# Kernel tuning notes

Measured on AMD Instinct MI355X. Metric: run time of the kernel, lower is better.

## Reference

```python
import jax, jax.numpy as jnp
import numpy as np

K_NEIGHBOURS = 40  # includes self; self is dropped after top-k


def setup_inputs() -> dict:
    key = jax.random.key(0)
    ks = jax.random.split(key, 4)
    B, V, F_in = 4, 4096, 64
    P, S, F_out = 64, 4, 64
    x = jax.random.normal(ks[0], (B, V, F_in), dtype=jnp.float32)
    Wf = jax.random.normal(ks[1], (F_in, P), dtype=jnp.float32) / np.sqrt(F_in)
    bf = jnp.zeros((P,), dtype=jnp.float32)
    Ws = jax.random.normal(ks[2], (F_in, S), dtype=jnp.float32) / np.sqrt(F_in)
    bs = jnp.zeros((S,), dtype=jnp.float32)
    Wo = jax.random.normal(ks[3], (F_in + 2 * P, F_out), dtype=jnp.float32) / np.sqrt(F_in + 2 * P)
    bo = jnpp = jnp.zeros((F_out,), dtype=jnp.float32)
    return {"x": x, "Wf": Wf, "bf": bf, "Ws": Ws, "bs": bs, "Wo": Wo, "bo": bo}


def _euclidean_squared(c):
    # c: [B, V, S] -> [B, V, V] squared pairwise distances
    sq = jnp.sum(c * c, axis=-1)  # [B, V]
    d2 = sq[:, :, None] + sq[:, None, :] - 2.0 * jnp.einsum('bvs,bus->bvu', c, c)
    return d2


def reference(x, Wf, bf, Ws, bs, Wo, bo):
    # learned spatial coordinates and propagated features
    coords = x @ Ws + bs            # [B, V, S]
    feats = x @ Wf + bf             # [B, V, P]

    d2 = _euclidean_squared(coords)                 # [B, V, V]
    neg_vals, idx = jax.lax.top_k(-d2, K_NEIGHBOURS)  # closest first (self at 0)
    nbr_idx = idx[:, :, 1:]                         # [B, V, K-1]
    dist = -neg_vals[:, :, 1:]                      # [B, V, K-1] (>= 0)

    # gauss_of_lin(d * 10) = exp(-|10 d|)
    w = jnp.exp(-jnp.abs(dist * 10.0))              # [B, V, K-1]

    # gather neighbour features per batch: [B, V, K-1, P]
    nf = jax.vmap(lambda f, i: f[i])(feats, nbr_idx)
    nf = nf * w[..., None]

    collected = jnp.concatenate([jnp.max(nf, axis=2), jnp.mean(nf, axis=2)], axis=-1)  # [B, V, 2P]
    updated = jnp.concatenate([x, collected], axis=-1)  # [B, V, F_in + 2P]
    return jnp.tanh(updated @ Wo + bo)
```

## Files before the change

### kernel.cpp

```cpp
#include <hip/hip_runtime.h>
#include <cmath>

#define BB  4
#define VV  4096
#define KK  40
#define FIN 64

typedef float v2f __attribute__((ext_vector_type(2)));

__global__ __launch_bounds__(256) void prep_kernel(
    const float* __restrict__ x, const float* __restrict__ Wf,
    const float* __restrict__ bf, const float* __restrict__ Ws,
    const float* __restrict__ bs,
    float* __restrict__ coords, float* __restrict__ sq,
    float* __restrict__ feats)
{
    int lane = threadIdx.x & 63;
    int wid  = threadIdx.x >> 6;
    int row0 = (blockIdx.x * 4 + wid) * 4;
    const float* xr = x + (size_t)row0 * FIN;

    float a0 = 0.f, a1 = 0.f, a2 = 0.f, a3 = 0.f;
    #pragma unroll 8
    for (int k = 0; k < FIN; ++k) {
        float wf = Wf[k * 64 + lane];
        a0 = fmaf(xr[k],        wf, a0);
        a1 = fmaf(xr[64  + k],  wf, a1);
        a2 = fmaf(xr[128 + k],  wf, a2);
        a3 = fmaf(xr[192 + k],  wf, a3);
    }
    float bfl = bf[lane];
    feats[(size_t)(row0 + 0) * 64 + lane] = a0 + bfl;
    feats[(size_t)(row0 + 1) * 64 + lane] = a1 + bfl;
    feats[(size_t)(row0 + 2) * 64 + lane] = a2 + bfl;
    feats[(size_t)(row0 + 3) * 64 + lane] = a3 + bfl;

    int r  = lane >> 4;
    int s  = (lane >> 2) & 3;
    int kc = lane & 3;
    const float* xrr = x + (size_t)(row0 + r) * FIN + kc * 16;
    const float* wsr = Ws + kc * 16 * 4 + s;
    float c = 0.f;
    #pragma unroll
    for (int k = 0; k < 16; ++k)
        c = fmaf(xrr[k], wsr[k * 4], c);
    c += __shfl_xor(c, 1, 64);
    c += __shfl_xor(c, 2, 64);
    float val = c + bs[s];
    if ((lane & 3) == 0) coords[(size_t)(row0 + r) * 4 + s] = val;
    float p = val * val;
    p += __shfl_xor(p, 4, 64);
    p += __shfl_xor(p, 8, 64);
    if ((lane & 15) == 0) sq[row0 + r] = p;
}

__global__ __launch_bounds__(256, 8) void gravnet_kernel(
    const float* __restrict__ x, const float* __restrict__ coords,
    const float* __restrict__ sq, const float* __restrict__ feats,
    const float* __restrict__ Wo, const float* __restrict__ bo,
    float* __restrict__ out)
{
    int lane = threadIdx.x & 63;
    int wid  = threadIdx.x >> 6;
    int q0   = (blockIdx.x * 4 + wid) * 2;
    int b    = q0 >> 12;
    int v0   = q0 & (VV - 1);

    __shared__ uint2               s_nb[4][2][KK];
    __shared__ __align__(16) float s_upd[4][2][192];

    const float4* cb  = (const float4*)(coords + (size_t)b * VV * 4);
    const float*  sqb = sq + (size_t)b * VV;

    float4 cqa = cb[v0], cqb = cb[v0 + 1];
    v2f nx = (v2f){-2.f * cqa.x, -2.f * cqb.x};
    v2f ny = (v2f){-2.f * cqa.y, -2.f * cqb.y};
    v2f nz = (v2f){-2.f * cqa.z, -2.f * cqb.z};
    v2f nw = (v2f){-2.f * cqa.w, -2.f * cqb.w};
    v2f hs = (v2f){sqb[v0], sqb[v0 + 1]};

    unsigned mm[2][4];
    #pragma unroll
    for (int qq = 0; qq < 2; ++qq)
        mm[qq][0] = mm[qq][1] = mm[qq][2] = mm[qq][3] = 0xFFFFFFFFu;

    #pragma unroll 4
    for (int i = 0; i < 64; ++i) {
        int u = i * 64 + lane;
        float4 cu = cb[u];
        float squ = cu.x * cu.x;
        squ = fmaf(cu.y, cu.y, squ);
        squ = fmaf(cu.z, cu.z, squ);
        squ = fmaf(cu.w, cu.w, squ);
        v2f acc = hs + (v2f){squ, squ};
        acc = __builtin_elementwise_fma(nx, (v2f){cu.x, cu.x}, acc);
        acc = __builtin_elementwise_fma(ny, (v2f){cu.y, cu.y}, acc);
        acc = __builtin_elementwise_fma(nz, (v2f){cu.z, cu.z}, acc);
        acc = __builtin_elementwise_fma(nw, (v2f){cu.w, cu.w}, acc);
        float d2s[2] = { acc.x, acc.y };
        #pragma unroll
        for (int qq = 0; qq < 2; ++qq) {
            float d2 = fmaxf(d2s[qq], 0.f);
            unsigned key = (__float_as_uint(d2) & 0xFFFFF000u) | (unsigned)u;
            unsigned b0 = max(mm[qq][0], key);
            unsigned b1 = max(mm[qq][1], key);
            unsigned b2 = max(mm[qq][2], key);
            mm[qq][0] = min(mm[qq][0], key);
            mm[qq][1] = min(mm[qq][1], b0);
            mm[qq][2] = min(mm[qq][2], b1);
            mm[qq][3] = min(mm[qq][3], b2);
        }
    }

    unsigned M[2] = {0u, 0u};
    for (int bit = 30; bit >= 0; --bit) {
        #pragma unroll
        for (int qq = 0; qq < 2; ++qq) {
            unsigned cand = M[qq] | (1u << bit);
            int cnt = (int)__popcll(__ballot(mm[qq][0] < cand))
                    + (int)__popcll(__ballot(mm[qq][1] < cand))
                    + (int)__popcll(__ballot(mm[qq][2] < cand))
                    + (int)__popcll(__ballot(mm[qq][3] < cand));
            if (cnt <= 39) M[qq] = cand;
        }
    }

    #pragma unroll
    for (int qq = 0; qq < 2; ++qq) {
        unsigned mn = mm[qq][0];
        #pragma unroll
        for (int off = 32; off >= 1; off >>= 1) {
            unsigned o = __shfl_xor(mn, off, 64);
            mn = o < mn ? o : mn;
        }
        int base = 0;
        #pragma unroll
        for (int i = 0; i < 4; ++i) {
            unsigned kk = mm[qq][i];
            bool pred = (kk <= M[qq]) && (kk != mn);
            unsigned long long mask = __ballot(pred);
            unsigned pos = (unsigned)base +
                __builtin_amdgcn_mbcnt_hi((unsigned)(mask >> 32),
                    __builtin_amdgcn_mbcnt_lo((unsigned)mask, 0u));
            if (pred) {
                float d2a = __uint_as_float(kk & 0xFFFFF000u);
                float w   = __expf(-10.f * d2a);
                s_nb[wid][qq][pos] =
                    make_uint2((kk & 4095u) << 8, __float_as_uint(w));
            }
            base += (int)__popcll(mask);
        }
    }

    const float* fb  = feats + (size_t)b * VV * 64;
    const char*  fbl = (const char*)(fb + lane);
    float vmax[2], vsum[2];
    #pragma unroll
    for (int qq = 0; qq < 2; ++qq) { vmax[qq] = -INFINITY; vsum[qq] = 0.f; }
    #pragma unroll 6
    for (int j = 0; j < KK - 1; ++j) {
        #pragma unroll
        for (int qq = 0; qq < 2; ++qq) {
            uint2 nb = s_nb[wid][qq][j];
            float f  = *(const float*)(fbl + nb.x);
            float w  = __uint_as_float(nb.y);
            float val = w * f;
            vmax[qq] = fmaxf(vmax[qq], val);
            vsum[qq] += val;
        }
    }

    #pragma unroll
    for (int qq = 0; qq < 2; ++qq) {
        s_upd[wid][qq][lane]       = x[(size_t)(q0 + qq) * 64 + lane];
        s_upd[wid][qq][64  + lane] = vmax[qq];
        s_upd[wid][qq][128 + lane] = vsum[qq] * (1.0f / 39.0f);
    }

    float bol = bo[lane];
    float acc0 = bol, acc1 = bol;
    #pragma unroll 4
    for (int j4 = 0; j4 < 48; ++j4) {
        float wo0 = Wo[(j4 * 4 + 0) * 64 + lane];
        float wo1 = Wo[(j4 * 4 + 1) * 64 + lane];
        float wo2 = Wo[(j4 * 4 + 2) * 64 + lane];
        float wo3 = Wo[(j4 * 4 + 3) * 64 + lane];
        float4 u0 = *(const float4*)&s_upd[wid][0][j4 * 4];
        float4 u1 = *(const float4*)&s_upd[wid][1][j4 * 4];
        acc0 = fmaf(u0.x, wo0, acc0);  acc1 = fmaf(u1.x, wo0, acc1);
        acc0 = fmaf(u0.y, wo1, acc0);  acc1 = fmaf(u1.y, wo1, acc1);
        acc0 = fmaf(u0.z, wo2, acc0);  acc1 = fmaf(u1.z, wo2, acc1);
        acc0 = fmaf(u0.w, wo3, acc0);  acc1 = fmaf(u1.w, wo3, acc1);
    }
    float e0 = __expf(2.f * acc0);
    float e1 = __expf(2.f * acc1);
    out[(size_t)q0 * 64 + lane]       = 1.f - __fdividef(2.f, e0 + 1.f);
    out[(size_t)(q0 + 1) * 64 + lane] = 1.f - __fdividef(2.f, e1 + 1.f);
}

extern "C" void kernel_launch(void* const* d_in, const int* in_sizes, int n_in,
                              void* d_out, int out_size, void* d_ws, size_t ws_size,
                              hipStream_t stream)
{
    (void)in_sizes; (void)n_in; (void)out_size; (void)ws_size;
    const float* x  = (const float*)d_in[0];
    const float* Wf = (const float*)d_in[1];
    const float* bf = (const float*)d_in[2];
    const float* Ws = (const float*)d_in[3];
    const float* bs = (const float*)d_in[4];
    const float* Wo = (const float*)d_in[5];
    const float* bo = (const float*)d_in[6];
    float* out = (float*)d_out;

    float* coords = (float*)d_ws;
    float* sq     = coords + (size_t)BB * VV * 4;
    float* feats  = sq + (size_t)BB * VV;

    prep_kernel<<<BB * VV / 16, 256, 0, stream>>>(x, Wf, bf, Ws, bs,
                                                  coords, sq, feats);
    gravnet_kernel<<<BB * VV / 8, 256, 0, stream>>>(x, coords, sq, feats,
                                                    Wo, bo, out);
}
```

Before: 133.1 us.

## Shorten radix threshold search and overlap second query's search with first gather

The per-query threshold bisection now searches only bits 30..12 and checks whether the 4096-wide bucket holds exactly 40 keys, falling back to the low 12 bits otherwise. Query 1's bisection steps are interleaved into query 0's neighbour-gather loop so ballot work overlaps global loads. The squared norm of each candidate is read from the precomputed sq buffer instead of being recomputed. The cost is more code and branches plus an extra load per candidate in the distance loop, traded for less ALU and cross-lane ballot latency.

```diff
diff --git a/kernel.cpp b/kernel.cpp
--- a/kernel.cpp
+++ b/kernel.cpp
@@ -88,10 +88,7 @@
     for (int i = 0; i < 64; ++i) {
         int u = i * 64 + lane;
         float4 cu = cb[u];
-        float squ = cu.x * cu.x;
-        squ = fmaf(cu.y, cu.y, squ);
-        squ = fmaf(cu.z, cu.z, squ);
-        squ = fmaf(cu.w, cu.w, squ);
+        float squ = sqb[u];
         v2f acc = hs + (v2f){squ, squ};
         acc = __builtin_elementwise_fma(nx, (v2f){cu.x, cu.x}, acc);
         acc = __builtin_elementwise_fma(ny, (v2f){cu.y, cu.y}, acc);
@@ -112,21 +109,20 @@
         }
     }
 
-    unsigned M[2] = {0u, 0u};
-    for (int bit = 30; bit >= 0; --bit) {
-        #pragma unroll
-        for (int qq = 0; qq < 2; ++qq) {
-            unsigned cand = M[qq] | (1u << bit);
-            int cnt = (int)__popcll(__ballot(mm[qq][0] < cand))
-                    + (int)__popcll(__ballot(mm[qq][1] < cand))
-                    + (int)__popcll(__ballot(mm[qq][2] < cand))
-                    + (int)__popcll(__ballot(mm[qq][3] < cand));
-            if (cnt <= 39) M[qq] = cand;
-        }
-    }
-
-    #pragma unroll
-    for (int qq = 0; qq < 2; ++qq) {
+    auto cnt_lt = [&](int qq, unsigned cand) -> int {
+        return (int)__popcll(__ballot(mm[qq][0] < cand))
+             + (int)__popcll(__ballot(mm[qq][1] < cand))
+             + (int)__popcll(__ballot(mm[qq][2] < cand))
+             + (int)__popcll(__ballot(mm[qq][3] < cand));
+    };
+    auto fallback12 = [&](int qq, unsigned& M) {
+        #pragma unroll
+        for (int bit = 11; bit >= 0; --bit) {
+            unsigned cand = M | (1u << bit);
+            if (cnt_lt(qq, cand) <= 39) M = cand;
+        }
+    };
+    auto compact = [&](int qq, unsigned Msel) {
         unsigned mn = mm[qq][0];
         #pragma unroll
         for (int off = 32; off >= 1; off >>= 1) {
@@ -137,7 +133,7 @@
         #pragma unroll
         for (int i = 0; i < 4; ++i) {
             unsigned kk = mm[qq][i];
-            bool pred = (kk <= M[qq]) && (kk != mn);
+            bool pred = (kk <= Msel) && (kk != mn);
             unsigned long long mask = __ballot(pred);
             unsigned pos = (unsigned)base +
                 __builtin_amdgcn_mbcnt_hi((unsigned)(mask >> 32),
@@ -150,32 +146,54 @@
             }
             base += (int)__popcll(mask);
         }
-    }
-
-    const float* fb  = feats + (size_t)b * VV * 64;
-    const char*  fbl = (const char*)(fb + lane);
-    float vmax[2], vsum[2];
-    #pragma unroll
-    for (int qq = 0; qq < 2; ++qq) { vmax[qq] = -INFINITY; vsum[qq] = 0.f; }
-    #pragma unroll 6
+    };
+
+    unsigned M0 = 0u;
+    #pragma unroll
+    for (int bit = 30; bit >= 12; --bit) {
+        unsigned cand = M0 | (1u << bit);
+        if (cnt_lt(0, cand) <= 39) M0 = cand;
+    }
+    unsigned Msel0 = M0 | 0xFFFu;
+    if (cnt_lt(0, M0 + 4096u) != 40) { fallback12(0, M0); Msel0 = M0; }
+    compact(0, Msel0);
+
+    const float* fb   = feats + (size_t)b * VV * 64;
+    unsigned     ln4  = (unsigned)lane * 4u;
+    float vmax0 = -INFINITY, vsum0 = 0.f;
+    unsigned M1 = 0u;
+    #pragma unroll
     for (int j = 0; j < KK - 1; ++j) {
-        #pragma unroll
-        for (int qq = 0; qq < 2; ++qq) {
-            uint2 nb = s_nb[wid][qq][j];
-            float f  = *(const float*)(fbl + nb.x);
-            float w  = __uint_as_float(nb.y);
-            float val = w * f;
-            vmax[qq] = fmaxf(vmax[qq], val);
-            vsum[qq] += val;
-        }
-    }
-
-    #pragma unroll
-    for (int qq = 0; qq < 2; ++qq) {
-        s_upd[wid][qq][lane]       = x[(size_t)(q0 + qq) * 64 + lane];
-        s_upd[wid][qq][64  + lane] = vmax[qq];
-        s_upd[wid][qq][128 + lane] = vsum[qq] * (1.0f / 39.0f);
-    }
+        uint2 nb = s_nb[wid][0][j];
+        float f  = *(const float*)((const char*)fb + (nb.x + ln4));
+        float val = __uint_as_float(nb.y) * f;
+        vmax0 = fmaxf(vmax0, val);
+        vsum0 += val;
+        if (j < 19) {
+            unsigned cand = M1 | (1u << (30 - j));
+            if (cnt_lt(1, cand) <= 39) M1 = cand;
+        }
+    }
+    unsigned Msel1 = M1 | 0xFFFu;
+    if (cnt_lt(1, M1 + 4096u) != 40) { fallback12(1, M1); Msel1 = M1; }
+    compact(1, Msel1);
+
+    float vmax1 = -INFINITY, vsum1 = 0.f;
+    #pragma unroll
+    for (int j = 0; j < KK - 1; ++j) {
+        uint2 nb = s_nb[wid][1][j];
+        float f  = *(const float*)((const char*)fb + (nb.x + ln4));
+        float val = __uint_as_float(nb.y) * f;
+        vmax1 = fmaxf(vmax1, val);
+        vsum1 += val;
+    }
+
+    s_upd[wid][0][lane]       = x[(size_t)q0 * 64 + lane];
+    s_upd[wid][0][64  + lane] = vmax0;
+    s_upd[wid][0][128 + lane] = vsum0 * (1.0f / 39.0f);
+    s_upd[wid][1][lane]       = x[(size_t)(q0 + 1) * 64 + lane];
+    s_upd[wid][1][64  + lane] = vmax1;
+    s_upd[wid][1][128 + lane] = vsum1 * (1.0f / 39.0f);
 
     float bol = bo[lane];
     float acc0 = bol, acc1 = bol;
```

After: 155.2 us. +16.6%, slower.
